# Kernel tuning notes

Measured on AMD Instinct MI355X. Metric: run time of the kernel, lower is better.

## Reference

```python
import jax, jax.numpy as jnp
import numpy as np
import math

H = 80; W = 80
FOVX = math.pi / 2.0; FOVY = math.pi / 2.0
TANX = math.tan(FOVX * 0.5); TANY = math.tan(FOVY * 0.5)
FOCAL_X = W / (2.0 * TANX); FOCAL_Y = H / (2.0 * TANY)
SCALE_MOD = 1.0
N_GAUSS = 4096; K_GEOM = 1024; K_SH = 1024

SH_C0 = 0.28209479177387814
SH_C1 = 0.4886025119029199
C2 = [1.0925484305920792, -1.0925484305920792, 0.31539156525252005, -1.0925484305920792, 0.5462742152960396]
C3 = [-0.5900435899266435, 2.890611442640554, -0.4570457994644658, 0.3731763325901154, -0.4570457994644658, 1.445305721320277, -0.5900435899266435]


def eval_sh3(sh, d):
    # sh: [N,16,3], d: [N,3] unit view directions -> clamped RGB [N,3]
    x, y, z = d[:, 0:1], d[:, 1:2], d[:, 2:3]
    xx, yy, zz = x * x, y * y, z * z
    xy, yz, xz = x * y, y * z, x * z
    res = (SH_C0 * sh[:, 0]
           - SH_C1 * y * sh[:, 1] + SH_C1 * z * sh[:, 2] - SH_C1 * x * sh[:, 3]
           + C2[0] * xy * sh[:, 4] + C2[1] * yz * sh[:, 5]
           + C2[2] * (2.0 * zz - xx - yy) * sh[:, 6]
           + C2[3] * xz * sh[:, 7] + C2[4] * (xx - yy) * sh[:, 8]
           + C3[0] * y * (3.0 * xx - yy) * sh[:, 9] + C3[1] * xy * z * sh[:, 10]
           + C3[2] * y * (4.0 * zz - xx - yy) * sh[:, 11]
           + C3[3] * z * (2.0 * zz - 3.0 * xx - 3.0 * yy) * sh[:, 12]
           + C3[4] * x * (4.0 * zz - xx - yy) * sh[:, 13]
           + C3[5] * z * (xx - yy) * sh[:, 14]
           + C3[6] * x * (xx - yy - 3.0 * zz) * sh[:, 15])
    return jnp.maximum(res + 0.5, 0.0)


def quat_to_rotmat(q):
    # q: [N,4] normalized (w,x,y,z) -> [N,3,3]
    w, x, y, z = q[:, 0], q[:, 1], q[:, 2], q[:, 3]
    r0 = jnp.stack([1 - 2 * (y * y + z * z), 2 * (x * y - w * z), 2 * (x * z + w * y)], -1)
    r1 = jnp.stack([2 * (x * y + w * z), 1 - 2 * (x * x + z * z), 2 * (y * z - w * x)], -1)
    r2 = jnp.stack([2 * (x * z - w * y), 2 * (y * z + w * x), 1 - 2 * (x * x + y * y)], -1)
    return jnp.stack([r0, r1, r2], axis=1)


def _forward(means3D, sh, sh_indices, g_indices, opacities, scales, scale_factors, rotations, extrinsic, bg):
    N = means3D.shape[0]
    # row-vector convention as in the torch wrapper: p_hom = [x,y,z,1] @ view
    R3 = extrinsic[:3, :3]; t3 = extrinsic[3, :3]
    p_view = means3D @ R3 + t3  # [N,3] camera space
    tx, ty, tz = p_view[:, 0], p_view[:, 1], p_view[:, 2]
    in_front = tz > 0.2  # near-plane cull as in CUDA kernel
    tz_s = jnp.where(in_front, tz, 1.0)
    # NDC (projection matrix reduces to x/(z tanx), y/(z tany)) then ndc2Pix
    gx = ((tx / (tz_s * TANX) + 1.0) * W - 1.0) * 0.5
    gy = ((ty / (tz_s * TANY) + 1.0) * H - 1.0) * 0.5
    # indexed 3D covariance: Sigma = R diag(s^2) R^T, codebook gathers
    s = scales[g_indices] * scale_factors * SCALE_MOD  # [N,3]
    q = rotations[g_indices]
    q = q / jnp.linalg.norm(q, axis=1, keepdims=True)
    Rm = quat_to_rotmat(q)
    cov3D = jnp.einsum('nij,nj,nkj->nik', Rm, s * s, Rm)
    # EWA splat: world->cam rotation is R3^T under row-vector storage
    Wm = R3.T
    cov_cam = jnp.einsum('ij,njk,lk->nil', Wm, cov3D, Wm)
    limx = 1.3 * TANX; limy = 1.3 * TANY
    txc = jnp.clip(tx / tz_s, -limx, limx) * tz_s
    tyc = jnp.clip(ty / tz_s, -limy, limy) * tz_s
    J = jnp.zeros((N, 2, 3), means3D.dtype)
    J = J.at[:, 0, 0].set(FOCAL_X / tz_s).at[:, 0, 2].set(-FOCAL_X * txc / (tz_s * tz_s))
    J = J.at[:, 1, 1].set(FOCAL_Y / tz_s).at[:, 1, 2].set(-FOCAL_Y * tyc / (tz_s * tz_s))
    cov2d = jnp.einsum('nij,njk,nlk->nil', J, cov_cam, J)
    a = cov2d[:, 0, 0] + 0.3; b = cov2d[:, 0, 1]; c = cov2d[:, 1, 1] + 0.3
    det = a * c - b * b
    valid = in_front & (det > 0)
    det_s = jnp.where(det != 0, det, 1.0)
    ca = c / det_s; cb = -b / det_s; cc = a / det_s  # conic
    mid = 0.5 * (a + c)
    lam1 = mid + jnp.sqrt(jnp.maximum(0.1, mid * mid - det))
    radii = jnp.where(valid, jnp.ceil(3.0 * jnp.sqrt(lam1)), 0.0).astype(jnp.int32)
    # SH -> RGB, view dir from camera position (extrinsic.inverse()[3,:3])
    campos = jnp.linalg.inv(extrinsic)[3, :3]
    dirs = means3D - campos
    dirs = dirs / jnp.linalg.norm(dirs, axis=1, keepdims=True)
    color = eval_sh3(sh[sh_indices], dirs)  # [N,3]
    # global front-to-back depth sort
    depth = jnp.where(valid, tz, jnp.inf)
    order = jnp.argsort(depth)
    gx_s, gy_s = gx[order], gy[order]
    ca_s, cb_s, cc_s = ca[order], cb[order], cc[order]
    op_s = opacities[order, 0]; col_s = color[order]; val_s = valid[order]
    # pixel grid (pixel centers at integer coords as in renderCUDA)
    ys, xs = jnp.meshgrid(jnp.arange(H, dtype=means3D.dtype), jnp.arange(W, dtype=means3D.dtype), indexing='ij')
    px = xs.reshape(-1); py = ys.reshape(-1)  # [P]
    dx = gx_s[None, :] - px[:, None]  # [P,N]
    dy = gy_s[None, :] - py[:, None]
    power = -0.5 * (ca_s * dx * dx + cc_s * dy * dy) - cb_s * dx * dy
    alpha = jnp.minimum(0.99, op_s[None, :] * jnp.exp(jnp.minimum(power, 0.0)))
    keep = (power <= 0.0) & val_s[None, :] & (alpha >= 1.0 / 255.0)
    alpha = jnp.where(keep, alpha, 0.0)
    om = 1.0 - alpha
    T_inc = jnp.cumprod(om, axis=1)
    inc = T_inc >= 1e-4  # early-termination prefix (T monotone)
    T_excl = jnp.concatenate([jnp.ones((px.shape[0], 1), om.dtype), T_inc[:, :-1]], axis=1)
    w = alpha * T_excl * inc
    T_final = jnp.prod(jnp.where(inc, om, 1.0), axis=1)
    out = w @ col_s + T_final[:, None] * bg[None, :]  # [P,3]
    color_img = jnp.transpose(out.reshape(H, W, 3), (2, 0, 1))  # [3,H,W]
    return color_img, radii


def setup_inputs() -> dict:
    key = jax.random.key(0)
    ks = jax.random.split(key, 9)
    xy = (jax.random.uniform(ks[0], (N_GAUSS, 2)) - 0.5) * 4.0
    z = jax.random.uniform(ks[1], (N_GAUSS, 1)) * 4.0 + 2.0
    means3D = jnp.concatenate([xy, z], axis=1)  # inside the view frustum
    sh = jax.random.normal(ks[2], (K_SH, 16, 3)) * 0.3
    sh_indices = jax.random.randint(ks[3], (N_GAUSS,), 0, K_SH)
    g_indices = jax.random.randint(ks[4], (N_GAUSS,), 0, K_GEOM)
    opacities = jax.random.uniform(ks[5], (N_GAUSS, 1), minval=0.1, maxval=0.99)
    scales = jax.random.uniform(ks[6], (K_GEOM, 3), minval=0.01, maxval=0.08)
    scale_factors = jax.random.uniform(ks[7], (N_GAUSS, 1), minval=0.5, maxval=1.5)
    rotations = jax.random.normal(ks[8], (K_GEOM, 4))
    extrinsic = jnp.eye(4, dtype=jnp.float32)
    bg = jnp.zeros((3,), jnp.float32)
    return dict(means3D=means3D, sh=sh, sh_indices=sh_indices, g_indices=g_indices,
                opacities=opacities, scales=scales, scale_factors=scale_factors,
                rotations=rotations, extrinsic=extrinsic, bg=bg)


def reference(means3D, sh, sh_indices, g_indices, opacities, scales, scale_factors, rotations, extrinsic, bg):
    return _forward(means3D, sh, sh_indices, g_indices, opacities, scales, scale_factors, rotations, extrinsic, bg)
```

## Files before the change

kernel.cpp:

```cpp
#include <hip/hip_runtime.h>
#include <math.h>

#define NG 4096
#define WI 80
#define HI 80
#define NPIX (WI*HI)
#define FOCAL 40.0f
#define LIM 1.3f
#define CAP 1024

#define SH_C0 0.28209479177387814f
#define SH_C1 0.4886025119029199f


__global__ __launch_bounds__(512) void tile_k(
    const float* __restrict__ means, const float* __restrict__ sh,
    const int* __restrict__ shidx, const int* __restrict__ gidx,
    const float* __restrict__ opac, const float* __restrict__ scales,
    const float* __restrict__ sfac, const float* __restrict__ rots,
    const float* __restrict__ ext, const float* __restrict__ bg,
    float* __restrict__ out)
{
  __shared__ unsigned long long kds[CAP];
  __shared__ float pr[CAP][9];
  __shared__ float pT[8][64], pR[8][64], pG[8][64], pB[8][64];
  __shared__ int scnt;
  int tid = threadIdx.x;
  if (tid == 0) scnt = 0;
  __syncthreads();

  int tile = blockIdx.x;
  int x0 = (tile % 10) * 8, y0 = (tile / 10) * 8;
  float bx0 = (float)x0, bx1 = (float)(x0 + 7);
  float by0 = (float)y0, by1 = (float)(y0 + 7);

  float e0=ext[0],  e1=ext[1],  e2=ext[2];
  float e4=ext[4],  e5=ext[5],  e6=ext[6];
  float e8=ext[8],  e9=ext[9],  e10=ext[10];
  float e12=ext[12], e13=ext[13], e14=ext[14];
  float cp0 = -(e12*e0 + e13*e1 + e14*e2);
  float cp1 = -(e12*e4 + e13*e5 + e14*e6);
  float cp2 = -(e12*e8 + e13*e9 + e14*e10);

  for (int c = 0; c < NG/512; ++c) {
    int g = c*512 + tid;
    float m0 = means[3*g+0], m1 = means[3*g+1], m2 = means[3*g+2];
    float tx = m0*e0 + m1*e4 + m2*e8  + e12;
    float ty = m0*e1 + m1*e5 + m2*e9  + e13;
    float tz = m0*e2 + m1*e6 + m2*e10 + e14;
    bool infront = tz > 0.2f;
    float tzs = infront ? tz : 1.0f;
    float inv_tzs = 1.0f / tzs;
    float gx = ((tx*inv_tzs + 1.0f)*WI - 1.0f)*0.5f;
    float gy = ((ty*inv_tzs + 1.0f)*HI - 1.0f)*0.5f;

    int gi = gidx[g];
    float sf = sfac[g];
    float s0 = scales[3*gi+0]*sf, s1 = scales[3*gi+1]*sf, s2 = scales[3*gi+2]*sf;
    float qw = rots[4*gi+0], qx = rots[4*gi+1], qy = rots[4*gi+2], qz = rots[4*gi+3];
    float qinv = rsqrtf(qw*qw+qx*qx+qy*qy+qz*qz);
    qw*=qinv; qx*=qinv; qy*=qinv; qz*=qinv;
    float r00 = 1.0f - 2.0f*(qy*qy+qz*qz);
    float r01 = 2.0f*(qx*qy - qw*qz);
    float r02 = 2.0f*(qx*qz + qw*qy);
    float r10 = 2.0f*(qx*qy + qw*qz);
    float r11 = 1.0f - 2.0f*(qx*qx+qz*qz);
    float r12 = 2.0f*(qy*qz - qw*qx);
    float r20 = 2.0f*(qx*qz - qw*qy);
    float r21 = 2.0f*(qy*qz + qw*qx);
    float r22 = 1.0f - 2.0f*(qx*qx+qy*qy);
    float v0 = s0*s0, v1 = s1*s1, v2 = s2*s2;
    float C00 = r00*r00*v0 + r01*r01*v1 + r02*r02*v2;
    float C01 = r00*r10*v0 + r01*r11*v1 + r02*r12*v2;
    float C02 = r00*r20*v0 + r01*r21*v1 + r02*r22*v2;
    float C11 = r10*r10*v0 + r11*r11*v1 + r12*r12*v2;
    float C12 = r10*r20*v0 + r11*r21*v1 + r12*r22*v2;
    float C22 = r20*r20*v0 + r21*r21*v1 + r22*r22*v2;
    float W0x=e0, W0y=e4, W0z=e8;
    float W1x=e1, W1y=e5, W1z=e9;
    float W2x=e2, W2y=e6, W2z=e10;
    float B00 = W0x*C00 + W0y*C01 + W0z*C02;
    float B01 = W0x*C01 + W0y*C11 + W0z*C12;
    float B02 = W0x*C02 + W0y*C12 + W0z*C22;
    float B10 = W1x*C00 + W1y*C01 + W1z*C02;
    float B11 = W1x*C01 + W1y*C11 + W1z*C12;
    float B12 = W1x*C02 + W1y*C12 + W1z*C22;
    float B20 = W2x*C00 + W2y*C01 + W2z*C02;
    float B21 = W2x*C01 + W2y*C11 + W2z*C12;
    float B22 = W2x*C02 + W2y*C12 + W2z*C22;
    float V00 = B00*W0x + B01*W0y + B02*W0z;
    float V01 = B00*W1x + B01*W1y + B02*W1z;
    float V02 = B00*W2x + B01*W2y + B02*W2z;
    float V11 = B10*W1x + B11*W1y + B12*W1z;
    float V12 = B10*W2x + B11*W2y + B12*W2z;
    float V22 = B20*W2x + B21*W2y + B22*W2z;
    float txz = tx*inv_tzs, tyz = ty*inv_tzs;
    float txc = fminf(fmaxf(txz, -LIM), LIM) * tzs;
    float tyc = fminf(fmaxf(tyz, -LIM), LIM) * tzs;
    float jx  = FOCAL*inv_tzs;
    float jy  = FOCAL*inv_tzs;
    float jz0 = -FOCAL*txc*inv_tzs*inv_tzs;
    float jz1 = -FOCAL*tyc*inv_tzs*inv_tzs;
    float c00 = jx*jx*V00 + 2.0f*jx*jz0*V02 + jz0*jz0*V22;
    float c01 = jx*jy*V01 + jx*jz1*V02 + jz0*jy*V12 + jz0*jz1*V22;
    float c11 = jy*jy*V11 + 2.0f*jy*jz1*V12 + jz1*jz1*V22;
    float a = c00 + 0.3f;
    float b = c01;
    float cf = c11 + 0.3f;
    float det = a*cf - b*b;
    bool valid = infront && (det > 0.0f);
    float dets = (det != 0.0f) ? det : 1.0f;
    float ca = cf/dets, cb = -b/dets, cc = a/dets;
    float mid = 0.5f*(a+cf);
    float lam1 = mid + sqrtf(fmaxf(0.1f, mid*mid - det));
    float radf = valid ? ceilf(3.0f*sqrtf(lam1)) : 0.0f;
    if (blockIdx.x == 0) out[3*NPIX + g] = radf;

    float op = valid ? opac[g] : 0.0f;
    float rc = valid ? sqrtf(fmaxf(0.0f, 2.0f*logf(255.0f*op))*lam1) + 0.01f : 0.0f;
    float nx = fminf(fmaxf(gx, bx0), bx1) - gx;
    float ny = fminf(fmaxf(gy, by0), by1) - gy;
    bool hit = (rc > 0.0f) && (nx*nx + ny*ny <= rc*rc);
    if (hit) {
      int slot = atomicAdd(&scnt, 1);
      if (slot < CAP) {
        float dx0 = m0-cp0, dy0 = m1-cp1, dz0 = m2-cp2;
        float dn = rsqrtf(dx0*dx0+dy0*dy0+dz0*dz0);
        float x = dx0*dn, y = dy0*dn, z = dz0*dn;
        float xx=x*x, yy=y*y, zz=z*z;
        float xy=x*y, yz=y*z, xz=x*z;
        float bf[16];
        bf[0]  = SH_C0;
        bf[1]  = -SH_C1*y;
        bf[2]  =  SH_C1*z;
        bf[3]  = -SH_C1*x;
        bf[4]  =  1.0925484305920792f*xy;
        bf[5]  = -1.0925484305920792f*yz;
        bf[6]  =  0.31539156525252005f*(2.0f*zz-xx-yy);
        bf[7]  = -1.0925484305920792f*xz;
        bf[8]  =  0.5462742152960396f*(xx-yy);
        bf[9]  = -0.5900435899266435f*y*(3.0f*xx-yy);
        bf[10] =  2.890611442640554f*xy*z;
        bf[11] = -0.4570457994644658f*y*(4.0f*zz-xx-yy);
        bf[12] =  0.3731763325901154f*z*(2.0f*zz-3.0f*xx-3.0f*yy);
        bf[13] = -0.4570457994644658f*x*(4.0f*zz-xx-yy);
        bf[14] =  1.445305721320277f*z*(xx-yy);
        bf[15] = -0.5900435899266435f*x*(xx-yy-3.0f*zz);
        const float* S = sh + (long)shidx[g]*48;
        float cr=0.f, cg=0.f, cbl=0.f;
        #pragma unroll
        for (int j=0;j<16;j++) {
          float w = bf[j];
          cr  += w*S[j*3+0];
          cg  += w*S[j*3+1];
          cbl += w*S[j*3+2];
        }
        cr  = fmaxf(cr +0.5f, 0.0f);
        cg  = fmaxf(cg +0.5f, 0.0f);
        cbl = fmaxf(cbl+0.5f, 0.0f);

        kds[slot] = ((unsigned long long)__float_as_uint(tz) << 22)
                  | ((unsigned long long)g << 10)
                  | (unsigned long long)slot;
        pr[slot][0]=gx; pr[slot][1]=gy;
        pr[slot][2]=ca; pr[slot][3]=cb; pr[slot][4]=cc;
        pr[slot][5]=op; pr[slot][6]=cr; pr[slot][7]=cg; pr[slot][8]=cbl;
      }
    }
  }
  __syncthreads();
  int cnt = scnt; if (cnt > CAP) cnt = CAP;

  int n = 1; while (n < cnt) n <<= 1;
  for (int i = tid; i < n; i += 512) if (i >= cnt) kds[i] = ~0ull;
  __syncthreads();
  for (int k = 2; k <= n; k <<= 1) {
    for (int j = k >> 1; j > 0; j >>= 1) {
      for (int i = tid; i < n; i += 512) {
        int l = i ^ j;
        if (l > i) {
          unsigned long long va = kds[i], vb = kds[l];
          bool asc = ((i & k) == 0);
          if ((va > vb) == asc) { kds[i] = vb; kds[l] = va; }
        }
      }
      __syncthreads();
    }
  }

  int wv = tid >> 6, lane = tid & 63;
  float px = (float)(x0 + (lane & 7));
  float py = (float)(y0 + (lane >> 3));
  int seg = (cnt + 7) >> 3;
  int s0i = wv*seg;
  int s1i = s0i + seg; if (s1i > cnt) s1i = cnt;
  float T = 1.0f, ar = 0.f, ag = 0.f, ab = 0.f;
  for (int e = s0i; e < s1i; ++e) {
    int slot = (int)(kds[e] & 1023ull);
    const float* q = pr[slot];
    float dx = q[0]-px, dy = q[1]-py;
    float power = -0.5f*(q[2]*dx*dx + q[4]*dy*dy) - q[3]*dx*dy;
    float al = 0.0f;
    if (power <= 0.0f) {
      float av = fminf(0.99f, q[5]*__expf(power));
      if (av >= (1.0f/255.0f)) al = av;
    }
    float w = al*T;
    ar += w*q[6]; ag += w*q[7]; ab += w*q[8];
    T *= 1.0f - al;
    if (__ballot(T >= 1e-4f) == 0ull) break;
  }
  pT[wv][lane]=T; pR[wv][lane]=ar; pG[wv][lane]=ag; pB[wv][lane]=ab;
  __syncthreads();

  if (tid < 64) {
    float Tg = 1.0f, r = 0.f, g2 = 0.f, b2 = 0.f;
    #pragma unroll
    for (int w = 0; w < 8; ++w) {
      r  += Tg*pR[w][tid];
      g2 += Tg*pG[w][tid];
      b2 += Tg*pB[w][tid];
      Tg *= pT[w][tid];
    }
    int p = (y0 + (tid>>3))*WI + (x0 + (tid&7));
    out[0*NPIX+p] = r  + Tg*bg[0];
    out[1*NPIX+p] = g2 + Tg*bg[1];
    out[2*NPIX+p] = b2 + Tg*bg[2];
  }
}

extern "C" void kernel_launch(void* const* d_in, const int* in_sizes, int n_in,
                              void* d_out, int out_size, void* d_ws, size_t ws_size,
                              hipStream_t stream) {
  const float* means  = (const float*)d_in[0];
  const float* sh     = (const float*)d_in[1];
  const int*   shidx  = (const int*)  d_in[2];
  const int*   gidx   = (const int*)  d_in[3];
  const float* opac   = (const float*)d_in[4];
  const float* scales = (const float*)d_in[5];
  const float* sfac   = (const float*)d_in[6];
  const float* rots   = (const float*)d_in[7];
  const float* ext    = (const float*)d_in[8];
  const float* bg     = (const float*)d_in[9];
  float* out = (float*)d_out;

  tile_k<<<100, 512, 0, stream>>>(means, sh, shidx, gidx, opac, scales, sfac,
                                  rots, ext, bg, out);
}
```

Measured before the change: 110.6 us.

## Split per-Gaussian preprocessing into a separate kernel and use rank sort

Moves the projection, covariance and SH colour work into a prep kernel that runs once per Gaussian and writes packed float4 records to the workspace. Before, each of the 100 tile blocks recomputed this for all 4096 Gaussians. The tile kernel now only culls against the tile using the precomputed centre and radius. It replaces the bitonic sort with an O(n^2) rank-counting sort and gathers the sorted records into shared SoA arrays. The cost is a second launch plus global round-trips, and the rank sort can become expensive when a tile has many hits.

```diff
diff --git a/kernel.cpp b/kernel.cpp
--- a/kernel.cpp
+++ b/kernel.cpp
@@ -12,17 +12,147 @@
 #define SH_C0 0.28209479177387814f
 #define SH_C1 0.4886025119029199f
 
-
-__global__ __launch_bounds__(512) void tile_k(
+__global__ __launch_bounds__(256) void prep_k(
     const float* __restrict__ means, const float* __restrict__ sh,
     const int* __restrict__ shidx, const int* __restrict__ gidx,
     const float* __restrict__ opac, const float* __restrict__ scales,
     const float* __restrict__ sfac, const float* __restrict__ rots,
-    const float* __restrict__ ext, const float* __restrict__ bg,
-    float* __restrict__ out)
+    const float* __restrict__ ext, float4* __restrict__ ws,
+    float* __restrict__ radii_out)
+{
+  int i = blockIdx.x*blockDim.x + threadIdx.x;
+  if (i >= NG) return;
+  float e0=ext[0],  e1=ext[1],  e2=ext[2];
+  float e4=ext[4],  e5=ext[5],  e6=ext[6];
+  float e8=ext[8],  e9=ext[9],  e10=ext[10];
+  float e12=ext[12], e13=ext[13], e14=ext[14];
+  float m0=means[3*i+0], m1=means[3*i+1], m2=means[3*i+2];
+  float tx = m0*e0 + m1*e4 + m2*e8  + e12;
+  float ty = m0*e1 + m1*e5 + m2*e9  + e13;
+  float tz = m0*e2 + m1*e6 + m2*e10 + e14;
+  bool infront = tz > 0.2f;
+  float tzs = infront ? tz : 1.0f;
+  float inv_tzs = 1.0f / tzs;
+  float gx = ((tx*inv_tzs + 1.0f)*WI - 1.0f)*0.5f;
+  float gy = ((ty*inv_tzs + 1.0f)*HI - 1.0f)*0.5f;
+
+  int gi = gidx[i];
+  float sf = sfac[i];
+  float s0 = scales[3*gi+0]*sf, s1 = scales[3*gi+1]*sf, s2 = scales[3*gi+2]*sf;
+  float qw = rots[4*gi+0], qx = rots[4*gi+1], qy = rots[4*gi+2], qz = rots[4*gi+3];
+  float qinv = rsqrtf(qw*qw+qx*qx+qy*qy+qz*qz);
+  qw*=qinv; qx*=qinv; qy*=qinv; qz*=qinv;
+  float r00 = 1.0f - 2.0f*(qy*qy+qz*qz);
+  float r01 = 2.0f*(qx*qy - qw*qz);
+  float r02 = 2.0f*(qx*qz + qw*qy);
+  float r10 = 2.0f*(qx*qy + qw*qz);
+  float r11 = 1.0f - 2.0f*(qx*qx+qz*qz);
+  float r12 = 2.0f*(qy*qz - qw*qx);
+  float r20 = 2.0f*(qx*qz - qw*qy);
+  float r21 = 2.0f*(qy*qz + qw*qx);
+  float r22 = 1.0f - 2.0f*(qx*qx+qy*qy);
+  float v0 = s0*s0, v1 = s1*s1, v2 = s2*s2;
+  float C00 = r00*r00*v0 + r01*r01*v1 + r02*r02*v2;
+  float C01 = r00*r10*v0 + r01*r11*v1 + r02*r12*v2;
+  float C02 = r00*r20*v0 + r01*r21*v1 + r02*r22*v2;
+  float C11 = r10*r10*v0 + r11*r11*v1 + r12*r12*v2;
+  float C12 = r10*r20*v0 + r11*r21*v1 + r12*r22*v2;
+  float C22 = r20*r20*v0 + r21*r21*v1 + r22*r22*v2;
+  float W0x=e0, W0y=e4, W0z=e8;
+  float W1x=e1, W1y=e5, W1z=e9;
+  float W2x=e2, W2y=e6, W2z=e10;
+  float B00 = W0x*C00 + W0y*C01 + W0z*C02;
+  float B01 = W0x*C01 + W0y*C11 + W0z*C12;
+  float B02 = W0x*C02 + W0y*C12 + W0z*C22;
+  float B10 = W1x*C00 + W1y*C01 + W1z*C02;
+  float B11 = W1x*C01 + W1y*C11 + W1z*C12;
+  float B12 = W1x*C02 + W1y*C12 + W1z*C22;
+  float B20 = W2x*C00 + W2y*C01 + W2z*C02;
+  float B21 = W2x*C01 + W2y*C11 + W2z*C12;
+  float B22 = W2x*C02 + W2y*C12 + W2z*C22;
+  float V00 = B00*W0x + B01*W0y + B02*W0z;
+  float V01 = B00*W1x + B01*W1y + B02*W1z;
+  float V02 = B00*W2x + B01*W2y + B02*W2z;
+  float V11 = B10*W1x + B11*W1y + B12*W1z;
+  float V12 = B10*W2x + B11*W2y + B12*W2z;
+  float V22 = B20*W2x + B21*W2y + B22*W2z;
+  float txz = tx*inv_tzs, tyz = ty*inv_tzs;
+  float txc = fminf(fmaxf(txz, -LIM), LIM) * tzs;
+  float tyc = fminf(fmaxf(tyz, -LIM), LIM) * tzs;
+  float jx  = FOCAL*inv_tzs;
+  float jy  = FOCAL*inv_tzs;
+  float jz0 = -FOCAL*txc*inv_tzs*inv_tzs;
+  float jz1 = -FOCAL*tyc*inv_tzs*inv_tzs;
+  float c00 = jx*jx*V00 + 2.0f*jx*jz0*V02 + jz0*jz0*V22;
+  float c01 = jx*jy*V01 + jx*jz1*V02 + jz0*jy*V12 + jz0*jz1*V22;
+  float c11 = jy*jy*V11 + 2.0f*jy*jz1*V12 + jz1*jz1*V22;
+  float a = c00 + 0.3f;
+  float b = c01;
+  float cf = c11 + 0.3f;
+  float det = a*cf - b*b;
+  bool valid = infront && (det > 0.0f);
+  float dets = (det != 0.0f) ? det : 1.0f;
+  float ca = cf/dets, cb = -b/dets, cc = a/dets;
+  float mid = 0.5f*(a+cf);
+  float lam1 = mid + sqrtf(fmaxf(0.1f, mid*mid - det));
+  float radf = valid ? ceilf(3.0f*sqrtf(lam1)) : 0.0f;
+  radii_out[i] = radf;
+
+  float op = valid ? opac[i] : 0.0f;
+  float rc = valid ? sqrtf(fmaxf(0.0f, 2.0f*logf(255.0f*op))*lam1) + 0.01f : 0.0f;
+
+  float cp0 = -(e12*e0 + e13*e1 + e14*e2);
+  float cp1 = -(e12*e4 + e13*e5 + e14*e6);
+  float cp2 = -(e12*e8 + e13*e9 + e14*e10);
+  float dx0 = m0-cp0, dy0 = m1-cp1, dz0 = m2-cp2;
+  float dn = rsqrtf(dx0*dx0+dy0*dy0+dz0*dz0);
+  float x = dx0*dn, y = dy0*dn, z = dz0*dn;
+  float xx=x*x, yy=y*y, zz=z*z;
+  float xy=x*y, yz=y*z, xz=x*z;
+  float bf[16];
+  bf[0]  = SH_C0;
+  bf[1]  = -SH_C1*y;
+  bf[2]  =  SH_C1*z;
+  bf[3]  = -SH_C1*x;
+  bf[4]  =  1.0925484305920792f*xy;
+  bf[5]  = -1.0925484305920792f*yz;
+  bf[6]  =  0.31539156525252005f*(2.0f*zz-xx-yy);
+  bf[7]  = -1.0925484305920792f*xz;
+  bf[8]  =  0.5462742152960396f*(xx-yy);
+  bf[9]  = -0.5900435899266435f*y*(3.0f*xx-yy);
+  bf[10] =  2.890611442640554f*xy*z;
+  bf[11] = -0.4570457994644658f*y*(4.0f*zz-xx-yy);
+  bf[12] =  0.3731763325901154f*z*(2.0f*zz-3.0f*xx-3.0f*yy);
+  bf[13] = -0.4570457994644658f*x*(4.0f*zz-xx-yy);
+  bf[14] =  1.445305721320277f*z*(xx-yy);
+  bf[15] = -0.5900435899266435f*x*(xx-yy-3.0f*zz);
+  const float* S = sh + (long)shidx[i]*48;
+  float cr=0.f, cg=0.f, cbl=0.f;
+  #pragma unroll
+  for (int j=0;j<16;j++) {
+    float w = bf[j];
+    cr  += w*S[j*3+0];
+    cg  += w*S[j*3+1];
+    cbl += w*S[j*3+2];
+  }
+  cr  = fmaxf(cr +0.5f, 0.0f);
+  cg  = fmaxf(cg +0.5f, 0.0f);
+  cbl = fmaxf(cbl+0.5f, 0.0f);
+
+  ws[i]        = make_float4(gx, gy, rc, infront ? tz : __builtin_inff());
+  ws[NG + i]   = make_float4(ca, cb, cc, op);
+  ws[2*NG + i] = make_float4(cr, cg, cbl, 0.0f);
+}
+
+__global__ __launch_bounds__(512) void tile_k(const float4* __restrict__ ws,
+                                              const float* __restrict__ bg,
+                                              float* __restrict__ out)
 {
   __shared__ unsigned long long kds[CAP];
-  __shared__ float pr[CAP][9];
+  __shared__ int   sidx[CAP];
+  __shared__ float2 sgxy[CAP];
+  __shared__ float4 sabc[CAP];
+  __shared__ float4 scol[CAP];
   __shared__ float pT[8][64], pR[8][64], pG[8][64], pB[8][64];
   __shared__ int scnt;
   int tid = threadIdx.x;
@@ -31,162 +161,39 @@
 
   int tile = blockIdx.x;
   int x0 = (tile % 10) * 8, y0 = (tile / 10) * 8;
-  float bx0 = (float)x0, bx1 = (float)(x0 + 7);
-  float by0 = (float)y0, by1 = (float)(y0 + 7);
-
-  float e0=ext[0],  e1=ext[1],  e2=ext[2];
-  float e4=ext[4],  e5=ext[5],  e6=ext[6];
-  float e8=ext[8],  e9=ext[9],  e10=ext[10];
-  float e12=ext[12], e13=ext[13], e14=ext[14];
-  float cp0 = -(e12*e0 + e13*e1 + e14*e2);
-  float cp1 = -(e12*e4 + e13*e5 + e14*e6);
-  float cp2 = -(e12*e8 + e13*e9 + e14*e10);
+  float bx0 = (float)x0, bx1 = (float)(x0+7);
+  float by0 = (float)y0, by1 = (float)(y0+7);
 
   for (int c = 0; c < NG/512; ++c) {
     int g = c*512 + tid;
-    float m0 = means[3*g+0], m1 = means[3*g+1], m2 = means[3*g+2];
-    float tx = m0*e0 + m1*e4 + m2*e8  + e12;
-    float ty = m0*e1 + m1*e5 + m2*e9  + e13;
-    float tz = m0*e2 + m1*e6 + m2*e10 + e14;
-    bool infront = tz > 0.2f;
-    float tzs = infront ? tz : 1.0f;
-    float inv_tzs = 1.0f / tzs;
-    float gx = ((tx*inv_tzs + 1.0f)*WI - 1.0f)*0.5f;
-    float gy = ((ty*inv_tzs + 1.0f)*HI - 1.0f)*0.5f;
-
-    int gi = gidx[g];
-    float sf = sfac[g];
-    float s0 = scales[3*gi+0]*sf, s1 = scales[3*gi+1]*sf, s2 = scales[3*gi+2]*sf;
-    float qw = rots[4*gi+0], qx = rots[4*gi+1], qy = rots[4*gi+2], qz = rots[4*gi+3];
-    float qinv = rsqrtf(qw*qw+qx*qx+qy*qy+qz*qz);
-    qw*=qinv; qx*=qinv; qy*=qinv; qz*=qinv;
-    float r00 = 1.0f - 2.0f*(qy*qy+qz*qz);
-    float r01 = 2.0f*(qx*qy - qw*qz);
-    float r02 = 2.0f*(qx*qz + qw*qy);
-    float r10 = 2.0f*(qx*qy + qw*qz);
-    float r11 = 1.0f - 2.0f*(qx*qx+qz*qz);
-    float r12 = 2.0f*(qy*qz - qw*qx);
-    float r20 = 2.0f*(qx*qz - qw*qy);
-    float r21 = 2.0f*(qy*qz + qw*qx);
-    float r22 = 1.0f - 2.0f*(qx*qx+qy*qy);
-    float v0 = s0*s0, v1 = s1*s1, v2 = s2*s2;
-    float C00 = r00*r00*v0 + r01*r01*v1 + r02*r02*v2;
-    float C01 = r00*r10*v0 + r01*r11*v1 + r02*r12*v2;
-    float C02 = r00*r20*v0 + r01*r21*v1 + r02*r22*v2;
-    float C11 = r10*r10*v0 + r11*r11*v1 + r12*r12*v2;
-    float C12 = r10*r20*v0 + r11*r21*v1 + r12*r22*v2;
-    float C22 = r20*r20*v0 + r21*r21*v1 + r22*r22*v2;
-    float W0x=e0, W0y=e4, W0z=e8;
-    float W1x=e1, W1y=e5, W1z=e9;
-    float W2x=e2, W2y=e6, W2z=e10;
-    float B00 = W0x*C00 + W0y*C01 + W0z*C02;
-    float B01 = W0x*C01 + W0y*C11 + W0z*C12;
-    float B02 = W0x*C02 + W0y*C12 + W0z*C22;
-    float B10 = W1x*C00 + W1y*C01 + W1z*C02;
-    float B11 = W1x*C01 + W1y*C11 + W1z*C12;
-    float B12 = W1x*C02 + W1y*C12 + W1z*C22;
-    float B20 = W2x*C00 + W2y*C01 + W2z*C02;
-    float B21 = W2x*C01 + W2y*C11 + W2z*C12;
-    float B22 = W2x*C02 + W2y*C12 + W2z*C22;
-    float V00 = B00*W0x + B01*W0y + B02*W0z;
-    float V01 = B00*W1x + B01*W1y + B02*W1z;
-    float V02 = B00*W2x + B01*W2y + B02*W2z;
-    float V11 = B10*W1x + B11*W1y + B12*W1z;
-    float V12 = B10*W2x + B11*W2y + B12*W2z;
-    float V22 = B20*W2x + B21*W2y + B22*W2z;
-    float txz = tx*inv_tzs, tyz = ty*inv_tzs;
-    float txc = fminf(fmaxf(txz, -LIM), LIM) * tzs;
-    float tyc = fminf(fmaxf(tyz, -LIM), LIM) * tzs;
-    float jx  = FOCAL*inv_tzs;
-    float jy  = FOCAL*inv_tzs;
-    float jz0 = -FOCAL*txc*inv_tzs*inv_tzs;
-    float jz1 = -FOCAL*tyc*inv_tzs*inv_tzs;
-    float c00 = jx*jx*V00 + 2.0f*jx*jz0*V02 + jz0*jz0*V22;
-    float c01 = jx*jy*V01 + jx*jz1*V02 + jz0*jy*V12 + jz0*jz1*V22;
-    float c11 = jy*jy*V11 + 2.0f*jy*jz1*V12 + jz1*jz1*V22;
-    float a = c00 + 0.3f;
-    float b = c01;
-    float cf = c11 + 0.3f;
-    float det = a*cf - b*b;
-    bool valid = infront && (det > 0.0f);
-    float dets = (det != 0.0f) ? det : 1.0f;
-    float ca = cf/dets, cb = -b/dets, cc = a/dets;
-    float mid = 0.5f*(a+cf);
-    float lam1 = mid + sqrtf(fmaxf(0.1f, mid*mid - det));
-    float radf = valid ? ceilf(3.0f*sqrtf(lam1)) : 0.0f;
-    if (blockIdx.x == 0) out[3*NPIX + g] = radf;
-
-    float op = valid ? opac[g] : 0.0f;
-    float rc = valid ? sqrtf(fmaxf(0.0f, 2.0f*logf(255.0f*op))*lam1) + 0.01f : 0.0f;
-    float nx = fminf(fmaxf(gx, bx0), bx1) - gx;
-    float ny = fminf(fmaxf(gy, by0), by1) - gy;
-    bool hit = (rc > 0.0f) && (nx*nx + ny*ny <= rc*rc);
-    if (hit) {
+    float4 v = ws[g];
+    float nx = fminf(fmaxf(v.x, bx0), bx1) - v.x;
+    float ny = fminf(fmaxf(v.y, by0), by1) - v.y;
+    if (v.z > 0.0f && nx*nx + ny*ny <= v.z*v.z) {
       int slot = atomicAdd(&scnt, 1);
-      if (slot < CAP) {
-        float dx0 = m0-cp0, dy0 = m1-cp1, dz0 = m2-cp2;
-        float dn = rsqrtf(dx0*dx0+dy0*dy0+dz0*dz0);
-        float x = dx0*dn, y = dy0*dn, z = dz0*dn;
-        float xx=x*x, yy=y*y, zz=z*z;
-        float xy=x*y, yz=y*z, xz=x*z;
-        float bf[16];
-        bf[0]  = SH_C0;
-        bf[1]  = -SH_C1*y;
-        bf[2]  =  SH_C1*z;
-        bf[3]  = -SH_C1*x;
-        bf[4]  =  1.0925484305920792f*xy;
-        bf[5]  = -1.0925484305920792f*yz;
-        bf[6]  =  0.31539156525252005f*(2.0f*zz-xx-yy);
-        bf[7]  = -1.0925484305920792f*xz;
-        bf[8]  =  0.5462742152960396f*(xx-yy);
-        bf[9]  = -0.5900435899266435f*y*(3.0f*xx-yy);
-        bf[10] =  2.890611442640554f*xy*z;
-        bf[11] = -0.4570457994644658f*y*(4.0f*zz-xx-yy);
-        bf[12] =  0.3731763325901154f*z*(2.0f*zz-3.0f*xx-3.0f*yy);
-        bf[13] = -0.4570457994644658f*x*(4.0f*zz-xx-yy);
-        bf[14] =  1.445305721320277f*z*(xx-yy);
-        bf[15] = -0.5900435899266435f*x*(xx-yy-3.0f*zz);
-        const float* S = sh + (long)shidx[g]*48;
-        float cr=0.f, cg=0.f, cbl=0.f;
-        #pragma unroll
-        for (int j=0;j<16;j++) {
-          float w = bf[j];
-          cr  += w*S[j*3+0];
-          cg  += w*S[j*3+1];
-          cbl += w*S[j*3+2];
-        }
-        cr  = fmaxf(cr +0.5f, 0.0f);
-        cg  = fmaxf(cg +0.5f, 0.0f);
-        cbl = fmaxf(cbl+0.5f, 0.0f);
-
-        kds[slot] = ((unsigned long long)__float_as_uint(tz) << 22)
-                  | ((unsigned long long)g << 10)
-                  | (unsigned long long)slot;
-        pr[slot][0]=gx; pr[slot][1]=gy;
-        pr[slot][2]=ca; pr[slot][3]=cb; pr[slot][4]=cc;
-        pr[slot][5]=op; pr[slot][6]=cr; pr[slot][7]=cg; pr[slot][8]=cbl;
-      }
+      if (slot < CAP)
+        kds[slot] = ((unsigned long long)__float_as_uint(v.w) << 32) | (unsigned)g;
     }
   }
   __syncthreads();
   int cnt = scnt; if (cnt > CAP) cnt = CAP;
 
-  int n = 1; while (n < cnt) n <<= 1;
-  for (int i = tid; i < n; i += 512) if (i >= cnt) kds[i] = ~0ull;
-  __syncthreads();
-  for (int k = 2; k <= n; k <<= 1) {
-    for (int j = k >> 1; j > 0; j >>= 1) {
-      for (int i = tid; i < n; i += 512) {
-        int l = i ^ j;
-        if (l > i) {
-          unsigned long long va = kds[i], vb = kds[l];
-          bool asc = ((i & k) == 0);
-          if ((va > vb) == asc) { kds[i] = vb; kds[l] = va; }
-        }
-      }
-      __syncthreads();
-    }
-  }
+  for (int i = tid; i < cnt; i += 512) {
+    unsigned long long ki = kds[i];
+    int r = 0;
+    for (int j = 0; j < cnt; ++j) r += (kds[j] < ki);
+    sidx[r] = (int)(ki & 0xFFFFFFFFull);
+  }
+  __syncthreads();
+
+  for (int i = tid; i < cnt; i += 512) {
+    int g = sidx[i];
+    float4 v = ws[g];
+    sgxy[i] = make_float2(v.x, v.y);
+    sabc[i] = ws[NG + g];
+    scol[i] = ws[2*NG + g];
+  }
+  __syncthreads();
 
   int wv = tid >> 6, lane = tid & 63;
   float px = (float)(x0 + (lane & 7));
@@ -196,17 +203,18 @@
   int s1i = s0i + seg; if (s1i > cnt) s1i = cnt;
   float T = 1.0f, ar = 0.f, ag = 0.f, ab = 0.f;
   for (int e = s0i; e < s1i; ++e) {
-    int slot = (int)(kds[e] & 1023ull);
-    const float* q = pr[slot];
-    float dx = q[0]-px, dy = q[1]-py;
-    float power = -0.5f*(q[2]*dx*dx + q[4]*dy*dy) - q[3]*dx*dy;
+    float2 xyv = sgxy[e];
+    float4 q   = sabc[e];
+    float dx = xyv.x - px, dy = xyv.y - py;
+    float power = -0.5f*(q.x*dx*dx + q.z*dy*dy) - q.y*dx*dy;
     float al = 0.0f;
     if (power <= 0.0f) {
-      float av = fminf(0.99f, q[5]*__expf(power));
+      float av = fminf(0.99f, q.w*__expf(power));
       if (av >= (1.0f/255.0f)) al = av;
     }
+    float4 cl = scol[e];
     float w = al*T;
-    ar += w*q[6]; ag += w*q[7]; ab += w*q[8];
+    ar += w*cl.x; ag += w*cl.y; ab += w*cl.z;
     T *= 1.0f - al;
     if (__ballot(T >= 1e-4f) == 0ull) break;
   }
@@ -243,7 +251,9 @@
   const float* ext    = (const float*)d_in[8];
   const float* bg     = (const float*)d_in[9];
   float* out = (float*)d_out;
-
-  tile_k<<<100, 512, 0, stream>>>(means, sh, shidx, gidx, opac, scales, sfac,
-                                  rots, ext, bg, out);
+  float4* ws = (float4*)d_ws;
+
+  prep_k<<<NG/256, 256, 0, stream>>>(means, sh, shidx, gidx, opac, scales, sfac,
+                                     rots, ext, ws, out + 3*NPIX);
+  tile_k<<<100, 512, 0, stream>>>(ws, bg, out);
 }
```

Result: faster. 97.65 us (-11.7%).
